# Optimization experiments

Measured on AMD Instinct MI355X. Metric: run time of the kernel, lower is better.

## Reference

```python
import jax, jax.numpy as jnp
import numpy as np

NUM_HEADS = 16
EPS = 1e-6
ROPE_THETA = 10000.0


def _rmsnorm_fp32(x, w):
    # RMSNorm computed in fp32, scale by learned weight (per head_dim)
    xf = x.astype(jnp.float32)
    var = jnp.mean(xf * xf, axis=-1, keepdims=True)
    return (xf * jax.lax.rsqrt(var + EPS) * w.astype(jnp.float32)).astype(x.dtype)


def _rope_3d_angles(T, H, W, head_dim):
    # split head_dim across (t,h,w) axes; all parts even
    dh = 2 * ((head_dim // 3) // 2)
    dw = dh
    dt = head_dim - dh - dw

    def axis_ang(L, d):
        inv = 1.0 / (ROPE_THETA ** (jnp.arange(0, d, 2, dtype=jnp.float32) / d))
        return jnp.arange(L, dtype=jnp.float32)[:, None] * inv[None, :]  # [L, d//2]

    at = axis_ang(T, dt)  # [T, dt/2]
    ah = axis_ang(H, dh)  # [H, dh/2]
    aw = axis_ang(W, dw)  # [W, dw/2]
    # broadcast to [T,H,W, head_dim//2] then flatten to [N, head_dim//2]
    at_g = jnp.broadcast_to(at[:, None, None, :], (T, H, W, dt // 2))
    ah_g = jnp.broadcast_to(ah[None, :, None, :], (T, H, W, dh // 2))
    aw_g = jnp.broadcast_to(aw[None, None, :, :], (T, H, W, dw // 2))
    ang = jnp.concatenate([at_g, ah_g, aw_g], axis=-1).reshape(T * H * W, head_dim // 2)
    return jnp.cos(ang), jnp.sin(ang)


def _apply_rope(x, cos, sin):
    # x: [B,Hh,N,D]; cos/sin: [N, D/2]; interleaved complex-pair rotation
    xr = x[..., 0::2]
    xi = x[..., 1::2]
    c = cos[None, None, :, :]
    s = sin[None, None, :, :]
    out_r = xr * c - xi * s
    out_i = xr * s + xi * c
    return jnp.stack([out_r, out_i], axis=-1).reshape(x.shape)


def setup_inputs() -> dict:
    key = jax.random.key(0)
    ks = jax.random.split(key, 7)
    dim, hd = 2048, 128
    x = jax.random.normal(ks[0], (1, 2048, dim), dtype=jnp.float32)
    qkv_w = jax.random.normal(ks[1], (3 * dim, dim), dtype=jnp.float32) * (dim ** -0.5)
    qkv_b = jax.random.normal(ks[2], (3 * dim,), dtype=jnp.float32) * 0.02
    proj_w = jax.random.normal(ks[3], (dim, dim), dtype=jnp.float32) * (dim ** -0.5)
    proj_b = jax.random.normal(ks[4], (dim,), dtype=jnp.float32) * 0.02
    q_norm_w = jnp.ones((hd,), dtype=jnp.float32)
    k_norm_w = jnp.ones((hd,), dtype=jnp.float32)
    return {"x": x, "qkv_w": qkv_w, "qkv_b": qkv_b, "proj_w": proj_w,
            "proj_b": proj_b, "q_norm_w": q_norm_w, "k_norm_w": k_norm_w,
            "t_dim": 8, "h_dim": 16, "w_dim": 16}


def reference(x, qkv_w, qkv_b, proj_w, proj_b, q_norm_w, k_norm_w, t_dim, h_dim, w_dim):
    B, N, C = x.shape
    Hh = NUM_HEADS
    D = C // Hh
    scale = D ** -0.5
    # QKV projection (torch Linear: x @ W.T + b)
    qkv = x @ qkv_w.T + qkv_b                      # [B,N,3C]
    qkv = qkv.reshape(B, N, 3, Hh, D).transpose(2, 0, 3, 1, 4)  # [3,B,Hh,N,D]
    q, k, v = qkv[0], qkv[1], qkv[2]
    q = _rmsnorm_fp32(q, q_norm_w)
    k = _rmsnorm_fp32(k, k_norm_w)
    cos, sin = _rope_3d_angles(t_dim, h_dim, w_dim, D)
    q = _apply_rope(q, cos, sin)
    k = _apply_rope(k, cos, sin)
    # SDPA (non-causal)
    scores = jnp.einsum('bhqd,bhkd->bhqk', q, k) * scale
    attn = jax.nn.softmax(scores, axis=-1)
    out = jnp.einsum('bhqk,bhkd->bhqd', attn, v)   # [B,Hh,N,D]
    out = out.transpose(0, 2, 1, 3).reshape(B, N, C)
    return out @ proj_w.T + proj_b
```

## Files before the change

### kernel.cpp

```cpp
#include <hip/hip_runtime.h>
#include <hip/hip_bf16.h>
#include <cstdint>
#include <cstddef>

typedef __attribute__((ext_vector_type(8))) short bf16x8;
typedef __attribute__((ext_vector_type(4))) float f32x4;
typedef __attribute__((ext_vector_type(16))) float f32x16;

#define AS1 __attribute__((address_space(1)))
#define AS3 __attribute__((address_space(3)))

__device__ __forceinline__ void gload_lds16(const void* g, void* l) {
  __builtin_amdgcn_global_load_lds((const AS1 void*)g, (AS3 void*)l, 16, 0, 0);
}

__device__ __forceinline__ unsigned short f2bf(float x) {
  __hip_bfloat16 h = __float2bfloat16(x);
  return __builtin_bit_cast(unsigned short, h);
}
__device__ __forceinline__ float bf2f(unsigned short u) {
  return __builtin_bit_cast(float, (unsigned int)u << 16);
}
__device__ __forceinline__ unsigned cvtpk(float a, float b) {
  unsigned r;
  asm("v_cvt_pk_bf16_f32 %0, %1, %2" : "=v"(r) : "v"(a), "v"(b));
  return r;
}
__device__ __forceinline__ void pswap(unsigned& x, unsigned& y) {
  asm volatile("v_permlane32_swap_b32 %0, %1" : "+v"(x), "+v"(y));
}

__global__ __launch_bounds__(256) void k_cvt_bf16(const float* __restrict__ in,
                                                  unsigned short* __restrict__ out,
                                                  int n4) {
  int i = blockIdx.x * 256 + threadIdx.x;
  const int stride = gridDim.x * 256;
  for (; i < n4; i += stride) {
    float4 v = reinterpret_cast<const float4*>(in)[i];
    ushort4 o;
    o.x = f2bf(v.x); o.y = f2bf(v.y); o.z = f2bf(v.z); o.w = f2bf(v.w);
    reinterpret_cast<ushort4*>(out)[i] = o;
  }
}

__global__ __launch_bounds__(256) void k_rope_tab(float* __restrict__ cosT,
                                                  float* __restrict__ sinT,
                                                  const int* __restrict__ hdim,
                                                  const int* __restrict__ wdim) {
  int idx = blockIdx.x * 256 + threadIdx.x;
  if (idx >= 2048 * 64) return;
  const int n = idx >> 6, j = idx & 63;
  const int H = *hdim, W = *wdim;
  const int w = n % W;
  const int rem = n / W;
  const int h = rem % H;
  const int t = rem / H;
  float pos, i2, d;
  if (j < 22)      { pos = (float)t; i2 = (float)(2 * j);        d = 44.f; }
  else if (j < 43) { pos = (float)h; i2 = (float)(2 * (j - 22)); d = 42.f; }
  else             { pos = (float)w; i2 = (float)(2 * (j - 43)); d = 42.f; }
  const float ang = pos * powf(10000.0f, -i2 / d);
  cosT[idx] = cosf(ang);
  sinT[idx] = sinf(ang);
}

__global__ __launch_bounds__(256, 2) void k_gemmQKV(const unsigned short* __restrict__ A,
                                                    const unsigned short* __restrict__ B,
                                                    const float* __restrict__ bias,
                                                    unsigned short* __restrict__ C,
                                                    int M, int N, int K) {
  __shared__ __align__(16) char lds[81920];
  const int tid = threadIdx.x;
  const int lane = tid & 63;
  const int wid = tid >> 6;
  const int wr = wid >> 1, wc = wid & 1;

  const int xcd = blockIdx.x & 7;
  const int t = blockIdx.x >> 3;
  const int bx = xcd * 4 + (t & 3);
  const int by = t >> 2;
  const int row0 = by * 128, col0 = bx * 192;
  const int NT = K >> 5;

  auto stageA = [&](int kcol0, char* slot) {
#pragma unroll
    for (int r = 0; r < 2; ++r) {
      const int off = r * 4096 + tid * 16;
      const int pair = off >> 7;
      const int un = (off & 127) ^ ((pair & 7) << 4);
      const int grow = pair * 2 + (un >> 6);
      gload_lds16(A + (size_t)(row0 + grow) * K + kcol0 + ((un & 63) >> 1),
                  slot + r * 4096 + wid * 1024);
    }
  };
  auto stageB = [&](int kcol0, char* slot) {
#pragma unroll
    for (int r = 0; r < 3; ++r) {
      const int off = r * 4096 + tid * 16;
      const int pair = off >> 7;
      const int un = (off & 127) ^ ((pair & 7) << 4);
      const int grow = pair * 2 + (un >> 6);
      gload_lds16(B + (size_t)(col0 + grow) * K + kcol0 + ((un & 63) >> 1),
                  slot + r * 4096 + wid * 1024);
    }
  };
  auto frag = [&](const char* slot, int r, int kb) -> bf16x8 {
    return *reinterpret_cast<const bf16x8*>(
        slot + (r >> 1) * 128 + ((((r & 1) << 6) + kb) ^ (((r >> 1) & 7) << 4)));
  };

  f32x4 acc[4][6];
#pragma unroll
  for (int i = 0; i < 4; ++i)
#pragma unroll
    for (int j = 0; j < 6; ++j) acc[i][j] = (f32x4){0.f, 0.f, 0.f, 0.f};

#pragma unroll
  for (int p = 0; p < 3; ++p) {
    stageA(p * 32, lds + p * 8192);
    stageB(p * 32, lds + 32768 + p * 12288);
  }
  asm volatile("s_waitcnt vmcnt(10)" ::: "memory");
  __builtin_amdgcn_s_barrier();

  const int kb = (lane >> 4) << 4;
  for (int j = 0; j < NT; ++j) {
    const char* baseA = lds + (j & 3) * 8192;
    const char* baseB = lds + 32768 + (j & 3) * 12288;
    bf16x8 af[4], bq[6];
#pragma unroll
    for (int fr = 0; fr < 4; ++fr) af[fr] = frag(baseA, wr * 64 + fr * 16 + (lane & 15), kb);
#pragma unroll
    for (int fc = 0; fc < 6; ++fc) bq[fc] = frag(baseB, wc * 96 + fc * 16 + (lane & 15), kb);

    const int jp = j + 3;
    if (jp < NT) {
      stageA(jp * 32, lds + (jp & 3) * 8192);
      stageB(jp * 32, lds + 32768 + (jp & 3) * 12288);
      asm volatile("s_waitcnt vmcnt(10)" ::: "memory");
    } else if (j + 2 < NT) {
      asm volatile("s_waitcnt vmcnt(5)" ::: "memory");
    } else if (j + 1 < NT) {
      asm volatile("s_waitcnt vmcnt(0)" ::: "memory");
    }
    if (j + 1 < NT) __builtin_amdgcn_s_barrier();

    __builtin_amdgcn_s_setprio(1);
#pragma unroll
    for (int fr = 0; fr < 4; ++fr)
#pragma unroll
      for (int fc = 0; fc < 6; ++fc)
        acc[fr][fc] = __builtin_amdgcn_mfma_f32_16x16x32_bf16(af[fr], bq[fc], acc[fr][fc], 0, 0, 0);
    __builtin_amdgcn_s_setprio(0);
  }

#pragma unroll
  for (int fr = 0; fr < 4; ++fr)
#pragma unroll
    for (int fc = 0; fc < 6; ++fc) {
      const int col = col0 + wc * 96 + fc * 16 + (lane & 15);
      const float bv = bias[col];
#pragma unroll
      for (int jj = 0; jj < 4; ++jj) {
        const int row = row0 + wr * 64 + fr * 16 + (lane >> 4) * 4 + jj;
        C[(size_t)row * N + col] = f2bf(acc[fr][fc][jj] + bv);
      }
    }
}

__global__ __launch_bounds__(256, 2) void k_gemmProj(const unsigned short* __restrict__ A,
                                                     const unsigned short* __restrict__ B,
                                                     float* __restrict__ Cp,
                                                     int M, int N, int K, int KS) {
  __shared__ __align__(16) char lds[65536];
  const int tid = threadIdx.x;
  const int lane = tid & 63;
  const int wid = tid >> 6;
  const int wr = wid >> 1, wc = wid & 1;
  const int row0 = blockIdx.y * 128;
  const int col0 = blockIdx.x * 128;
  const int k0 = blockIdx.z * KS;
  const int NT = KS >> 5;

  auto stageS = [&](const unsigned short* src, int grow0, int kcol0, char* slot) {
#pragma unroll
    for (int r = 0; r < 2; ++r) {
      const int off = r * 4096 + tid * 16;
      const int pair = off >> 7;
      const int un = (off & 127) ^ ((pair & 7) << 4);
      const int grow = pair * 2 + (un >> 6);
      gload_lds16(src + (size_t)(grow0 + grow) * K + kcol0 + ((un & 63) >> 1),
                  slot + r * 4096 + wid * 1024);
    }
  };
  auto frag = [&](const char* slot, int r, int kb) -> bf16x8 {
    return *reinterpret_cast<const bf16x8*>(
        slot + (r >> 1) * 128 + ((((r & 1) << 6) + kb) ^ (((r >> 1) & 7) << 4)));
  };

  f32x4 acc[4][4];
#pragma unroll
  for (int i = 0; i < 4; ++i)
#pragma unroll
    for (int j = 0; j < 4; ++j) acc[i][j] = (f32x4){0.f, 0.f, 0.f, 0.f};

#pragma unroll
  for (int p = 0; p < 3; ++p) {
    stageS(A, row0, k0 + p * 32, lds + p * 8192);
    stageS(B, col0, k0 + p * 32, lds + 32768 + p * 8192);
  }
  asm volatile("s_waitcnt vmcnt(8)" ::: "memory");
  __builtin_amdgcn_s_barrier();

  const int kb = (lane >> 4) << 4;
  for (int j = 0; j < NT; ++j) {
    const char* baseA = lds + (j & 3) * 8192;
    const char* baseB = lds + 32768 + (j & 3) * 8192;
    bf16x8 af[4], bq[4];
#pragma unroll
    for (int fr = 0; fr < 4; ++fr) af[fr] = frag(baseA, wr * 64 + fr * 16 + (lane & 15), kb);
#pragma unroll
    for (int fc = 0; fc < 4; ++fc) bq[fc] = frag(baseB, wc * 64 + fc * 16 + (lane & 15), kb);

    const int jp = j + 3;
    if (jp < NT) {
      stageS(A, row0, k0 + jp * 32, lds + (jp & 3) * 8192);
      stageS(B, col0, k0 + jp * 32, lds + 32768 + (jp & 3) * 8192);
      asm volatile("s_waitcnt vmcnt(8)" ::: "memory");
    } else if (j + 2 < NT) {
      asm volatile("s_waitcnt vmcnt(4)" ::: "memory");
    } else if (j + 1 < NT) {
      asm volatile("s_waitcnt vmcnt(0)" ::: "memory");
    }
    if (j + 1 < NT) __builtin_amdgcn_s_barrier();

    __builtin_amdgcn_s_setprio(1);
#pragma unroll
    for (int fr = 0; fr < 4; ++fr)
#pragma unroll
      for (int fc = 0; fc < 4; ++fc)
        acc[fr][fc] = __builtin_amdgcn_mfma_f32_16x16x32_bf16(af[fr], bq[fc], acc[fr][fc], 0, 0, 0);
    __builtin_amdgcn_s_setprio(0);
  }

  float* Cz = Cp + (size_t)blockIdx.z * M * N;
#pragma unroll
  for (int fr = 0; fr < 4; ++fr)
#pragma unroll
    for (int fc = 0; fc < 4; ++fc) {
      const int col = col0 + wc * 64 + fc * 16 + (lane & 15);
#pragma unroll
      for (int jj = 0; jj < 4; ++jj) {
        const int row = row0 + wr * 64 + fr * 16 + (lane >> 4) * 4 + jj;
        Cz[(size_t)row * N + col] = acc[fr][fc][jj];
      }
    }
}

__global__ __launch_bounds__(256) void k_addbias(const float* __restrict__ Cp,
                                                 const float* __restrict__ bias,
                                                 float* __restrict__ out) {
  const int i = blockIdx.x * 256 + threadIdx.x;
  const float4 a = reinterpret_cast<const float4*>(Cp)[i];
  const float4 b = reinterpret_cast<const float4*>(Cp + 2048ull * 2048)[i];
  const float4 bv = reinterpret_cast<const float4*>(bias)[i & 511];
  float4 o;
  o.x = a.x + b.x + bv.x; o.y = a.y + b.y + bv.y;
  o.z = a.z + b.z + bv.z; o.w = a.w + b.w + bv.w;
  reinterpret_cast<float4*>(out)[i] = o;
}

__global__ __launch_bounds__(256) void k_qk_post(const unsigned short* __restrict__ qkv,
                                                 const float* __restrict__ qw,
                                                 const float* __restrict__ kw,
                                                 const float* __restrict__ cosT,
                                                 const float* __restrict__ sinT,
                                                 unsigned short* __restrict__ qo,
                                                 unsigned short* __restrict__ ko) {
  const int lane = threadIdx.x & 63;
  const int wid = threadIdx.x >> 6;
  const int pair = blockIdx.x * 4 + wid;
  const int n = pair >> 4, h = pair & 15;
  const float c = cosT[n * 64 + lane];
  const float s = sinT[n * 64 + lane];
#pragma unroll
  for (int sq = 0; sq < 2; ++sq) {
    const unsigned short* src = qkv + (size_t)n * 6144 + sq * 2048 + h * 128;
    const unsigned int vp = reinterpret_cast<const unsigned int*>(src)[lane];
    const float vx = bf2f((unsigned short)(vp & 0xffff));
    const float vy = bf2f((unsigned short)(vp >> 16));
    float ss = vx * vx + vy * vy;
#pragma unroll
    for (int m = 1; m < 64; m <<= 1) ss += __shfl_xor(ss, m, 64);
    const float r = rsqrtf(ss * (1.0f / 128.0f) + 1e-6f);
    float2 wv = reinterpret_cast<const float2*>(sq == 0 ? qw : kw)[lane];
    const float xr = vx * r * wv.x;
    const float xi = vy * r * wv.y;
    float orr = xr * c - xi * s;
    float oi  = xr * s + xi * c;
    if (sq == 0) { orr *= 0.08838834764831845f; oi *= 0.08838834764831845f; }
    unsigned short* dst = (sq == 0 ? qo : ko) + ((size_t)h * 2048 + n) * 128 + 2 * lane;
    const unsigned int pk = (unsigned int)f2bf(orr) | ((unsigned int)f2bf(oi) << 16);
    *reinterpret_cast<unsigned int*>(dst) = pk;
  }
}

__global__ __launch_bounds__(256) void k_v_tr(const unsigned short* __restrict__ qkv,
                                              unsigned short* __restrict__ vt2) {
  __shared__ __align__(16) unsigned short tile[64][136];
  const int h = blockIdx.y;
  const int n0 = blockIdx.x * 64;
  const int t = threadIdx.x;
  {
    const int row = t >> 2;
    const int c0 = (t & 3) * 32;
    const unsigned short* src = qkv + (size_t)(n0 + row) * 6144 + 4096 + h * 128 + c0;
#pragma unroll
    for (int j = 0; j < 32; j += 8)
      *reinterpret_cast<bf16x8*>(&tile[row][c0 + j]) =
          *reinterpret_cast<const bf16x8*>(src + j);
  }
  __syncthreads();
#pragma unroll
  for (int g4 = 0; g4 < 4; ++g4) {
    const int g = g4 * 256 + t;
    const int c = g >> 8;
    const int dblk = (g >> 6) & 3;
    const int p = g & 63;
    const int d = dblk * 32 + (p & 31);
    const int hi = p >> 5;
    bf16x8 o;
#pragma unroll
    for (int e = 0; e < 8; ++e) o[e] = (short)tile[c * 16 + hi * 8 + e][d];
    const size_t oidx = ((((size_t)h * 128 + (n0 >> 4) + c) * 4 + dblk) * 64 + p) * 8;
    *reinterpret_cast<bf16x8*>(vt2 + oidx) = o;
  }
}

__global__ __launch_bounds__(256) void k_fattn(const unsigned short* __restrict__ q,
                                               const unsigned short* __restrict__ k,
                                               const unsigned short* __restrict__ vt2,
                                               unsigned short* __restrict__ Onorm,
                                               float* __restrict__ lseb) {
  __shared__ __align__(16) unsigned short Ks[2][64 * 128];
  __shared__ __align__(16) unsigned short Vs[2][64 * 128];
  const int lane = threadIdx.x & 63;
  const int wid = threadIdx.x >> 6;
  const int hi2 = lane >> 5;
  const int ql = lane & 31;
  const int bid = blockIdx.x;
  const int h = bid & 15;
  const int qb = (bid >> 4) & 15;
  const int ksp = bid >> 8;
  const int q0 = qb * 128 + wid * 32;
  const int kbase = ksp * 1024;

  auto stageK = [&](int buf, int kt2) {
#pragma unroll
    for (int r = 0; r < 4; ++r) {
      const int off = r * 4096 + (wid * 64 + lane) * 16;
      const int row = off >> 8;
      const int colb = (off & 255) ^ ((row & 15) << 4);
      gload_lds16(k + ((size_t)h * 2048 + kbase + kt2 * 64 + row) * 128 + (colb >> 1),
                  (char*)Ks[buf] + r * 4096 + wid * 1024);
    }
  };
  auto stageV = [&](int buf, int kt2) {
    const unsigned short* vbase = vt2 + ((size_t)h * 128 + (kbase >> 4) + kt2 * 4) * 2048;
#pragma unroll
    for (int r = 0; r < 4; ++r)
      gload_lds16(vbase + r * 2048 + (wid * 64 + lane) * 8,
                  (char*)Vs[buf] + r * 4096 + wid * 1024);
  };

  bf16x8 qf[8];
  {
    const unsigned short* qp = q + ((size_t)h * 2048 + q0 + ql) * 128 + hi2 * 8;
#pragma unroll
    for (int c = 0; c < 8; ++c) qf[c] = *reinterpret_cast<const bf16x8*>(qp + c * 16);
  }
  f32x16 O[4];
#pragma unroll
  for (int i = 0; i < 4; ++i)
#pragma unroll
    for (int j = 0; j < 16; ++j) O[i][j] = 0.f;
  float m = -1e30f, l = 0.f;

  stageK(0, 0);
  stageV(0, 0);
  asm volatile("s_waitcnt vmcnt(0)" ::: "memory");
  __builtin_amdgcn_s_barrier();

  const int kswz = (lane & 15) << 4;
  for (int kt = 0; kt < 16; ++kt) {
    const int cur = kt & 1;
    const bool pf = (kt + 1 < 16);
    if (pf) { stageK(cur ^ 1, kt + 1); stageV(cur ^ 1, kt + 1); }

    f32x16 s0, s1;
#pragma unroll
    for (int j = 0; j < 16; ++j) { s0[j] = 0.f; s1[j] = 0.f; }
    __builtin_amdgcn_s_setprio(1);
#pragma unroll
    for (int c = 0; c < 8; ++c) {
      bf16x8 a0 = *reinterpret_cast<const bf16x8*>(
          (const char*)Ks[cur] + ql * 256 + ((c * 32 + hi2 * 16) ^ kswz));
      s0 = __builtin_amdgcn_mfma_f32_32x32x16_bf16(a0, qf[c], s0, 0, 0, 0);
    }
#pragma unroll
    for (int c = 0; c < 8; ++c) {
      bf16x8 a1 = *reinterpret_cast<const bf16x8*>(
          (const char*)Ks[cur] + (32 + ql) * 256 + ((c * 32 + hi2 * 16) ^ kswz));
      s1 = __builtin_amdgcn_mfma_f32_32x32x16_bf16(a1, qf[c], s1, 0, 0, 0);
    }
    __builtin_amdgcn_s_setprio(0);

    float mt = s0[0];
#pragma unroll
    for (int j = 1; j < 16; ++j) mt = fmaxf(mt, s0[j]);
#pragma unroll
    for (int j = 0; j < 16; ++j) mt = fmaxf(mt, s1[j]);
    mt = fmaxf(mt, __shfl_xor(mt, 32, 64));

    if (!__all(mt <= m + 8.0f)) {
      const float mn = fmaxf(m, mt);
      const float al = __expf(m - mn);
      m = mn;
      l *= al;
#pragma unroll
      for (int i = 0; i < 4; ++i)
#pragma unroll
        for (int j = 0; j < 16; ++j) O[i][j] *= al;
    }
    float rs = 0.f;
#pragma unroll
    for (int j = 0; j < 16; ++j) {
      s0[j] = __expf(s0[j] - m); rs += s0[j];
      s1[j] = __expf(s1[j] - m); rs += s1[j];
    }
    rs += __shfl_xor(rs, 32, 64);
    l += rs;

    bf16x8 pfr[4];
#pragma unroll
    for (int half = 0; half < 2; ++half) {
      const f32x16& sv = half ? s1 : s0;
      unsigned a[8];
#pragma unroll
      for (int j2 = 0; j2 < 8; ++j2) a[j2] = cvtpk(sv[2 * j2], sv[2 * j2 + 1]);
      pswap(a[0], a[2]);
      pswap(a[1], a[3]);
      pswap(a[4], a[6]);
      pswap(a[5], a[7]);
      union { uint4 u; bf16x8 v; } p0, p1;
      p0.u.x = a[0]; p0.u.y = a[1]; p0.u.z = a[2]; p0.u.w = a[3];
      p1.u.x = a[4]; p1.u.y = a[5]; p1.u.z = a[6]; p1.u.w = a[7];
      pfr[half * 2 + 0] = p0.v;
      pfr[half * 2 + 1] = p1.v;
    }

    __builtin_amdgcn_s_setprio(1);
#pragma unroll
    for (int dblk = 0; dblk < 4; ++dblk) {
#pragma unroll
      for (int c2 = 0; c2 < 4; ++c2) {
        bf16x8 va = *reinterpret_cast<const bf16x8*>(
            (const char*)Vs[cur] + ((c2 * 4 + dblk) * 64 + lane) * 16);
        O[dblk] = __builtin_amdgcn_mfma_f32_32x32x16_bf16(va, pfr[c2], O[dblk], 0, 0, 0);
      }
    }
    __builtin_amdgcn_s_setprio(0);

    if (pf) {
      asm volatile("s_waitcnt vmcnt(0)" ::: "memory");
      __builtin_amdgcn_s_barrier();
    }
  }

  const float rl = 1.0f / l;
  const int n = q0 + ql;
  unsigned short* ob = Onorm + (((size_t)(ksp * 16 + h) * 2048) + n) * 128;
#pragma unroll
  for (int dblk = 0; dblk < 4; ++dblk)
#pragma unroll
    for (int a = 0; a < 4; ++a) {
      uint2 w;
      w.x = (unsigned)f2bf(O[dblk][a * 4 + 0] * rl) | ((unsigned)f2bf(O[dblk][a * 4 + 1] * rl) << 16);
      w.y = (unsigned)f2bf(O[dblk][a * 4 + 2] * rl) | ((unsigned)f2bf(O[dblk][a * 4 + 3] * rl) << 16);
      *reinterpret_cast<uint2*>(ob + dblk * 32 + a * 8 + hi2 * 4) = w;
    }
  if (hi2 == 0)
    lseb[(size_t)(ksp * 16 + h) * 2048 + n] = m + logf(l);
}

__global__ __launch_bounds__(256) void k_merge(const unsigned short* __restrict__ Onorm,
                                               const float* __restrict__ lseb,
                                               unsigned short* __restrict__ att) {
  const int idx = blockIdx.x * 256 + threadIdx.x;
  const int n = idx >> 8;
  const int r = idx & 255;
  const int h = r >> 4;
  const int d0 = (r & 15) * 8;
  const float l0 = lseb[(size_t)h * 2048 + n];
  const float l1 = lseb[(size_t)(16 + h) * 2048 + n];
  const float M = fmaxf(l0, l1);
  float w0 = __expf(l0 - M), w1 = __expf(l1 - M);
  const float inv = 1.0f / (w0 + w1);
  w0 *= inv; w1 *= inv;
  const bf16x8 o0 = *reinterpret_cast<const bf16x8*>(
      Onorm + ((size_t)h * 2048 + n) * 128 + d0);
  const bf16x8 o1 = *reinterpret_cast<const bf16x8*>(
      Onorm + ((size_t)(16 + h) * 2048 + n) * 128 + d0);
  bf16x8 o;
#pragma unroll
  for (int e = 0; e < 8; ++e)
    o[e] = (short)f2bf(bf2f((unsigned short)o0[e]) * w0 + bf2f((unsigned short)o1[e]) * w1);
  *reinterpret_cast<bf16x8*>(att + (size_t)n * 2048 + h * 128 + d0) = o;
}

extern "C" void kernel_launch(void* const* d_in, const int* in_sizes, int n_in,
                              void* d_out, int out_size, void* d_ws, size_t ws_size,
                              hipStream_t stream) {
  (void)in_sizes; (void)n_in; (void)out_size; (void)ws_size;
  const float* x      = (const float*)d_in[0];
  const float* qkv_w  = (const float*)d_in[1];
  const float* qkv_b  = (const float*)d_in[2];
  const float* proj_w = (const float*)d_in[3];
  const float* proj_b = (const float*)d_in[4];
  const float* q_nw   = (const float*)d_in[5];
  const float* k_nw   = (const float*)d_in[6];
  const int* h_dim    = (const int*)d_in[8];
  const int* w_dim    = (const int*)d_in[9];
  float* out = (float*)d_out;

  char* ws = (char*)d_ws;
  size_t off = 0;
  auto carve = [&](size_t bytes) -> void* {
    void* p = ws + off;
    off += (bytes + 255) & ~(size_t)255;
    return p;
  };
  unsigned short* x_bf   = (unsigned short*)carve(2048ull * 2048 * 2);
  unsigned short* w1_bf  = (unsigned short*)carve(6144ull * 2048 * 2);
  unsigned short* w2_bf  = (unsigned short*)carve(2048ull * 2048 * 2);
  unsigned short* qkvb   = (unsigned short*)carve(2048ull * 6144 * 2);
  unsigned short* q_bf   = (unsigned short*)carve(16ull * 2048 * 128 * 2);
  unsigned short* k_bf   = (unsigned short*)carve(16ull * 2048 * 128 * 2);
  unsigned short* vt2_bf = (unsigned short*)carve(16ull * 2048 * 128 * 2);
  unsigned short* att_bf = (unsigned short*)carve(2048ull * 2048 * 2);
  unsigned short* on_bf  = (unsigned short*)carve(2ull * 16 * 2048 * 128 * 2);
  float*          lseb   = (float*)carve(2ull * 16 * 2048 * 4);
  float*          projp  = (float*)carve(2ull * 2048 * 2048 * 4);
  float*          cosT   = (float*)carve(2048ull * 64 * 4);
  float*          sinT   = (float*)carve(2048ull * 64 * 4);

  hipLaunchKernelGGL(k_cvt_bf16, dim3(2048), dim3(256), 0, stream, x, x_bf, 2048 * 2048 / 4);
  hipLaunchKernelGGL(k_cvt_bf16, dim3(2048), dim3(256), 0, stream, qkv_w, w1_bf, 6144 * 2048 / 4);
  hipLaunchKernelGGL(k_cvt_bf16, dim3(2048), dim3(256), 0, stream, proj_w, w2_bf, 2048 * 2048 / 4);
  hipLaunchKernelGGL(k_rope_tab, dim3(512), dim3(256), 0, stream, cosT, sinT, h_dim, w_dim);
  hipLaunchKernelGGL(k_gemmQKV, dim3(512), dim3(256), 0, stream,
                     x_bf, w1_bf, qkv_b, qkvb, 2048, 6144, 2048);
  hipLaunchKernelGGL(k_qk_post, dim3(8192), dim3(256), 0, stream,
                     qkvb, q_nw, k_nw, cosT, sinT, q_bf, k_bf);
  hipLaunchKernelGGL(k_v_tr, dim3(32, 16), dim3(256), 0, stream, qkvb, vt2_bf);
  hipLaunchKernelGGL(k_fattn, dim3(512), dim3(256), 0, stream,
                     q_bf, k_bf, vt2_bf, on_bf, lseb);
  hipLaunchKernelGGL(k_merge, dim3(2048), dim3(256), 0, stream, on_bf, lseb, att_bf);
  hipLaunchKernelGGL(k_gemmProj, dim3(16, 16, 2), dim3(256), 0, stream,
                     att_bf, w2_bf, projp, 2048, 2048, 2048, 1024);
  hipLaunchKernelGGL(k_addbias, dim3(4096), dim3(256), 0, stream, projp, proj_b, out);
}
```

Before: 179.1 us.

## Double-buffer MFMA fragments in registers to overlap LDS reads with compute

Both GEMM kernels (QKV and output projection) now keep two register sets of A/B fragments. The main loop is unrolled by two, so the LDS fragment reads for the next k-step are issued before the MFMAs of the current step. This is meant to hide LDS read latency behind matrix-core work. In exchange it roughly doubles the fragment register footprint, which could cut occupancy under launch_bounds(256,2), and the loop now assumes NT is even.

```diff
diff --git a/kernel.cpp b/kernel.cpp
--- a/kernel.cpp
+++ b/kernel.cpp
@@ -76,9 +76,9 @@
   const int wr = wid >> 1, wc = wid & 1;
 
   const int xcd = blockIdx.x & 7;
-  const int t = blockIdx.x >> 3;
-  const int bx = xcd * 4 + (t & 3);
-  const int by = t >> 2;
+  const int t0 = blockIdx.x >> 3;
+  const int bx = xcd * 4 + (t0 & 3);
+  const int by = t0 >> 2;
   const int row0 = by * 128, col0 = bx * 192;
   const int NT = K >> 5;
 
@@ -124,34 +124,69 @@
   __builtin_amdgcn_s_barrier();
 
   const int kb = (lane >> 4) << 4;
-  for (int j = 0; j < NT; ++j) {
-    const char* baseA = lds + (j & 3) * 8192;
-    const char* baseB = lds + 32768 + (j & 3) * 12288;
-    bf16x8 af[4], bq[6];
-#pragma unroll
-    for (int fr = 0; fr < 4; ++fr) af[fr] = frag(baseA, wr * 64 + fr * 16 + (lane & 15), kb);
-#pragma unroll
-    for (int fc = 0; fc < 6; ++fc) bq[fc] = frag(baseB, wc * 96 + fc * 16 + (lane & 15), kb);
-
-    const int jp = j + 3;
-    if (jp < NT) {
-      stageA(jp * 32, lds + (jp & 3) * 8192);
-      stageB(jp * 32, lds + 32768 + (jp & 3) * 12288);
-      asm volatile("s_waitcnt vmcnt(10)" ::: "memory");
-    } else if (j + 2 < NT) {
-      asm volatile("s_waitcnt vmcnt(5)" ::: "memory");
-    } else if (j + 1 < NT) {
-      asm volatile("s_waitcnt vmcnt(0)" ::: "memory");
-    }
-    if (j + 1 < NT) __builtin_amdgcn_s_barrier();
-
-    __builtin_amdgcn_s_setprio(1);
-#pragma unroll
-    for (int fr = 0; fr < 4; ++fr)
-#pragma unroll
-      for (int fc = 0; fc < 6; ++fc)
-        acc[fr][fc] = __builtin_amdgcn_mfma_f32_16x16x32_bf16(af[fr], bq[fc], acc[fr][fc], 0, 0, 0);
-    __builtin_amdgcn_s_setprio(0);
+  bf16x8 afA[4], bqA[6], afB[4], bqB[6];
+#pragma unroll
+  for (int fr = 0; fr < 4; ++fr) afA[fr] = frag(lds, wr * 64 + fr * 16 + (lane & 15), kb);
+#pragma unroll
+  for (int fc = 0; fc < 6; ++fc) bqA[fc] = frag(lds + 32768, wc * 96 + fc * 16 + (lane & 15), kb);
+
+  for (int j = 0; j < NT; j += 2) {
+    {
+      const int jp = j + 3;
+      if (jp < NT) {
+        stageA(jp * 32, lds + (jp & 3) * 8192);
+        stageB(jp * 32, lds + 32768 + (jp & 3) * 12288);
+        asm volatile("s_waitcnt vmcnt(10)" ::: "memory");
+      } else if (j + 2 < NT) {
+        asm volatile("s_waitcnt vmcnt(5)" ::: "memory");
+      } else {
+        asm volatile("s_waitcnt vmcnt(0)" ::: "memory");
+      }
+      __builtin_amdgcn_s_barrier();
+      const char* bA = lds + ((j + 1) & 3) * 8192;
+      const char* bB = lds + 32768 + ((j + 1) & 3) * 12288;
+#pragma unroll
+      for (int fr = 0; fr < 4; ++fr) afB[fr] = frag(bA, wr * 64 + fr * 16 + (lane & 15), kb);
+#pragma unroll
+      for (int fc = 0; fc < 6; ++fc) bqB[fc] = frag(bB, wc * 96 + fc * 16 + (lane & 15), kb);
+      __builtin_amdgcn_s_setprio(1);
+#pragma unroll
+      for (int fr = 0; fr < 4; ++fr)
+#pragma unroll
+        for (int fc = 0; fc < 6; ++fc)
+          acc[fr][fc] = __builtin_amdgcn_mfma_f32_16x16x32_bf16(afA[fr], bqA[fc], acc[fr][fc], 0, 0, 0);
+      __builtin_amdgcn_s_setprio(0);
+    }
+    {
+      const int t = j + 1;
+      const int jp = t + 3;
+      const bool more = (t + 1 < NT);
+      if (jp < NT) {
+        stageA(jp * 32, lds + (jp & 3) * 8192);
+        stageB(jp * 32, lds + 32768 + (jp & 3) * 12288);
+        asm volatile("s_waitcnt vmcnt(10)" ::: "memory");
+      } else if (t + 2 < NT) {
+        asm volatile("s_waitcnt vmcnt(5)" ::: "memory");
+      } else if (more) {
+        asm volatile("s_waitcnt vmcnt(0)" ::: "memory");
+      }
+      if (more) {
+        __builtin_amdgcn_s_barrier();
+        const char* bA = lds + ((t + 1) & 3) * 8192;
+        const char* bB = lds + 32768 + ((t + 1) & 3) * 12288;
+#pragma unroll
+        for (int fr = 0; fr < 4; ++fr) afA[fr] = frag(bA, wr * 64 + fr * 16 + (lane & 15), kb);
+#pragma unroll
+        for (int fc = 0; fc < 6; ++fc) bqA[fc] = frag(bB, wc * 96 + fc * 16 + (lane & 15), kb);
+      }
+      __builtin_amdgcn_s_setprio(1);
+#pragma unroll
+      for (int fr = 0; fr < 4; ++fr)
+#pragma unroll
+        for (int fc = 0; fc < 6; ++fc)
+          acc[fr][fc] = __builtin_amdgcn_mfma_f32_16x16x32_bf16(afB[fr], bqB[fc], acc[fr][fc], 0, 0, 0);
+      __builtin_amdgcn_s_setprio(0);
+    }
   }
 
 #pragma unroll
@@ -213,34 +248,69 @@
   __builtin_amdgcn_s_barrier();
 
   const int kb = (lane >> 4) << 4;
-  for (int j = 0; j < NT; ++j) {
-    const char* baseA = lds + (j & 3) * 8192;
-    const char* baseB = lds + 32768 + (j & 3) * 8192;
-    bf16x8 af[4], bq[4];
-#pragma unroll
-    for (int fr = 0; fr < 4; ++fr) af[fr] = frag(baseA, wr * 64 + fr * 16 + (lane & 15), kb);
-#pragma unroll
-    for (int fc = 0; fc < 4; ++fc) bq[fc] = frag(baseB, wc * 64 + fc * 16 + (lane & 15), kb);
-
-    const int jp = j + 3;
-    if (jp < NT) {
-      stageS(A, row0, k0 + jp * 32, lds + (jp & 3) * 8192);
-      stageS(B, col0, k0 + jp * 32, lds + 32768 + (jp & 3) * 8192);
-      asm volatile("s_waitcnt vmcnt(8)" ::: "memory");
-    } else if (j + 2 < NT) {
-      asm volatile("s_waitcnt vmcnt(4)" ::: "memory");
-    } else if (j + 1 < NT) {
-      asm volatile("s_waitcnt vmcnt(0)" ::: "memory");
-    }
-    if (j + 1 < NT) __builtin_amdgcn_s_barrier();
-
-    __builtin_amdgcn_s_setprio(1);
-#pragma unroll
-    for (int fr = 0; fr < 4; ++fr)
-#pragma unroll
-      for (int fc = 0; fc < 4; ++fc)
-        acc[fr][fc] = __builtin_amdgcn_mfma_f32_16x16x32_bf16(af[fr], bq[fc], acc[fr][fc], 0, 0, 0);
-    __builtin_amdgcn_s_setprio(0);
+  bf16x8 afA[4], bqA[4], afB[4], bqB[4];
+#pragma unroll
+  for (int fr = 0; fr < 4; ++fr) afA[fr] = frag(lds, wr * 64 + fr * 16 + (lane & 15), kb);
+#pragma unroll
+  for (int fc = 0; fc < 4; ++fc) bqA[fc] = frag(lds + 32768, wc * 64 + fc * 16 + (lane & 15), kb);
+
+  for (int j = 0; j < NT; j += 2) {
+    {
+      const int jp = j + 3;
+      if (jp < NT) {
+        stageS(A, row0, k0 + jp * 32, lds + (jp & 3) * 8192);
+        stageS(B, col0, k0 + jp * 32, lds + 32768 + (jp & 3) * 8192);
+        asm volatile("s_waitcnt vmcnt(8)" ::: "memory");
+      } else if (j + 2 < NT) {
+        asm volatile("s_waitcnt vmcnt(4)" ::: "memory");
+      } else {
+        asm volatile("s_waitcnt vmcnt(0)" ::: "memory");
+      }
+      __builtin_amdgcn_s_barrier();
+      const char* bA = lds + ((j + 1) & 3) * 8192;
+      const char* bB = lds + 32768 + ((j + 1) & 3) * 8192;
+#pragma unroll
+      for (int fr = 0; fr < 4; ++fr) afB[fr] = frag(bA, wr * 64 + fr * 16 + (lane & 15), kb);
+#pragma unroll
+      for (int fc = 0; fc < 4; ++fc) bqB[fc] = frag(bB, wc * 64 + fc * 16 + (lane & 15), kb);
+      __builtin_amdgcn_s_setprio(1);
+#pragma unroll
+      for (int fr = 0; fr < 4; ++fr)
+#pragma unroll
+        for (int fc = 0; fc < 4; ++fc)
+          acc[fr][fc] = __builtin_amdgcn_mfma_f32_16x16x32_bf16(afA[fr], bqA[fc], acc[fr][fc], 0, 0, 0);
+      __builtin_amdgcn_s_setprio(0);
+    }
+    {
+      const int t = j + 1;
+      const int jp = t + 3;
+      const bool more = (t + 1 < NT);
+      if (jp < NT) {
+        stageS(A, row0, k0 + jp * 32, lds + (jp & 3) * 8192);
+        stageS(B, col0, k0 + jp * 32, lds + 32768 + (jp & 3) * 8192);
+        asm volatile("s_waitcnt vmcnt(8)" ::: "memory");
+      } else if (t + 2 < NT) {
+        asm volatile("s_waitcnt vmcnt(4)" ::: "memory");
+      } else if (more) {
+        asm volatile("s_waitcnt vmcnt(0)" ::: "memory");
+      }
+      if (more) {
+        __builtin_amdgcn_s_barrier();
+        const char* bA = lds + ((t + 1) & 3) * 8192;
+        const char* bB = lds + 32768 + ((t + 1) & 3) * 8192;
+#pragma unroll
+        for (int fr = 0; fr < 4; ++fr) afA[fr] = frag(bA, wr * 64 + fr * 16 + (lane & 15), kb);
+#pragma unroll
+        for (int fc = 0; fc < 4; ++fc) bqA[fc] = frag(bB, wc * 64 + fc * 16 + (lane & 15), kb);
+      }
+      __builtin_amdgcn_s_setprio(1);
+#pragma unroll
+      for (int fr = 0; fr < 4; ++fr)
+#pragma unroll
+        for (int fc = 0; fc < 4; ++fc)
+          acc[fr][fc] = __builtin_amdgcn_mfma_f32_16x16x32_bf16(afB[fr], bqB[fc], acc[fr][fc], 0, 0, 0);
+      __builtin_amdgcn_s_setprio(0);
+    }
   }
 
   float* Cz = Cp + (size_t)blockIdx.z * M * N;
```

Result: no change. 178.4 us (-0.4%).

## Split attention keys four ways, single-buffer K tile, fuse weight conversions

Applied to the files above, without the earlier changes.

Flash attention now splits the key range into four 512-key chunks instead of two, doubling the grid to 1024 blocks, and the merge kernel combines four partial outputs using log-sum-exp weights. The K tile in shared memory becomes single-buffered, with a barrier after the QK MFMAs before prefetching the next tile. This lowers LDS use per block and may let more blocks share a CU. The three fp32-to-bf16 conversion launches are merged into one kernel. The cost is twice the partial-output traffic, a merge that reads twice as much, and K prefetch that can no longer overlap the QK compute.

```diff
diff --git a/kernel.cpp b/kernel.cpp
--- a/kernel.cpp
+++ b/kernel.cpp
@@ -30,16 +30,24 @@
   asm volatile("v_permlane32_swap_b32 %0, %1" : "+v"(x), "+v"(y));
 }
 
-__global__ __launch_bounds__(256) void k_cvt_bf16(const float* __restrict__ in,
-                                                  unsigned short* __restrict__ out,
-                                                  int n4) {
-  int i = blockIdx.x * 256 + threadIdx.x;
+__global__ __launch_bounds__(256) void k_cvt3(const float* __restrict__ a, unsigned short* __restrict__ ao, int na4,
+                                              const float* __restrict__ b, unsigned short* __restrict__ bo, int nb4,
+                                              const float* __restrict__ c, unsigned short* __restrict__ co, int nc4) {
   const int stride = gridDim.x * 256;
-  for (; i < n4; i += stride) {
-    float4 v = reinterpret_cast<const float4*>(in)[i];
-    ushort4 o;
-    o.x = f2bf(v.x); o.y = f2bf(v.y); o.z = f2bf(v.z); o.w = f2bf(v.w);
-    reinterpret_cast<ushort4*>(out)[i] = o;
+  for (int i = blockIdx.x * 256 + threadIdx.x; i < na4; i += stride) {
+    float4 v = reinterpret_cast<const float4*>(a)[i];
+    ushort4 o; o.x = f2bf(v.x); o.y = f2bf(v.y); o.z = f2bf(v.z); o.w = f2bf(v.w);
+    reinterpret_cast<ushort4*>(ao)[i] = o;
+  }
+  for (int i = blockIdx.x * 256 + threadIdx.x; i < nb4; i += stride) {
+    float4 v = reinterpret_cast<const float4*>(b)[i];
+    ushort4 o; o.x = f2bf(v.x); o.y = f2bf(v.y); o.z = f2bf(v.z); o.w = f2bf(v.w);
+    reinterpret_cast<ushort4*>(bo)[i] = o;
+  }
+  for (int i = blockIdx.x * 256 + threadIdx.x; i < nc4; i += stride) {
+    float4 v = reinterpret_cast<const float4*>(c)[i];
+    ushort4 o; o.x = f2bf(v.x); o.y = f2bf(v.y); o.z = f2bf(v.z); o.w = f2bf(v.w);
+    reinterpret_cast<ushort4*>(co)[i] = o;
   }
 }
 
@@ -76,9 +84,9 @@
   const int wr = wid >> 1, wc = wid & 1;
 
   const int xcd = blockIdx.x & 7;
-  const int t = blockIdx.x >> 3;
-  const int bx = xcd * 4 + (t & 3);
-  const int by = t >> 2;
+  const int t0 = blockIdx.x >> 3;
+  const int bx = xcd * 4 + (t0 & 3);
+  const int by = t0 >> 2;
   const int row0 = by * 128, col0 = bx * 192;
   const int NT = K >> 5;
 
@@ -342,7 +350,7 @@
                                                const unsigned short* __restrict__ vt2,
                                                unsigned short* __restrict__ Onorm,
                                                float* __restrict__ lseb) {
-  __shared__ __align__(16) unsigned short Ks[2][64 * 128];
+  __shared__ __align__(16) unsigned short Ks[64 * 128];
   __shared__ __align__(16) unsigned short Vs[2][64 * 128];
   const int lane = threadIdx.x & 63;
   const int wid = threadIdx.x >> 6;
@@ -353,16 +361,16 @@
   const int qb = (bid >> 4) & 15;
   const int ksp = bid >> 8;
   const int q0 = qb * 128 + wid * 32;
-  const int kbase = ksp * 1024;
-
-  auto stageK = [&](int buf, int kt2) {
+  const int kbase = ksp * 512;
+
+  auto stageK = [&](int kt2) {
 #pragma unroll
     for (int r = 0; r < 4; ++r) {
       const int off = r * 4096 + (wid * 64 + lane) * 16;
       const int row = off >> 8;
       const int colb = (off & 255) ^ ((row & 15) << 4);
       gload_lds16(k + ((size_t)h * 2048 + kbase + kt2 * 64 + row) * 128 + (colb >> 1),
-                  (char*)Ks[buf] + r * 4096 + wid * 1024);
+                  (char*)Ks + r * 4096 + wid * 1024);
     }
   };
   auto stageV = [&](int buf, int kt2) {
@@ -386,16 +394,15 @@
     for (int j = 0; j < 16; ++j) O[i][j] = 0.f;
   float m = -1e30f, l = 0.f;
 
-  stageK(0, 0);
+  stageK(0);
   stageV(0, 0);
   asm volatile("s_waitcnt vmcnt(0)" ::: "memory");
   __builtin_amdgcn_s_barrier();
 
   const int kswz = (lane & 15) << 4;
-  for (int kt = 0; kt < 16; ++kt) {
+  for (int kt = 0; kt < 8; ++kt) {
     const int cur = kt & 1;
-    const bool pf = (kt + 1 < 16);
-    if (pf) { stageK(cur ^ 1, kt + 1); stageV(cur ^ 1, kt + 1); }
+    const bool pf = (kt + 1 < 8);
 
     f32x16 s0, s1;
 #pragma unroll
@@ -404,16 +411,18 @@
 #pragma unroll
     for (int c = 0; c < 8; ++c) {
       bf16x8 a0 = *reinterpret_cast<const bf16x8*>(
-          (const char*)Ks[cur] + ql * 256 + ((c * 32 + hi2 * 16) ^ kswz));
+          (const char*)Ks + ql * 256 + ((c * 32 + hi2 * 16) ^ kswz));
       s0 = __builtin_amdgcn_mfma_f32_32x32x16_bf16(a0, qf[c], s0, 0, 0, 0);
     }
 #pragma unroll
     for (int c = 0; c < 8; ++c) {
       bf16x8 a1 = *reinterpret_cast<const bf16x8*>(
-          (const char*)Ks[cur] + (32 + ql) * 256 + ((c * 32 + hi2 * 16) ^ kswz));
+          (const char*)Ks + (32 + ql) * 256 + ((c * 32 + hi2 * 16) ^ kswz));
       s1 = __builtin_amdgcn_mfma_f32_32x32x16_bf16(a1, qf[c], s1, 0, 0, 0);
     }
     __builtin_amdgcn_s_setprio(0);
+    __builtin_amdgcn_s_barrier();
+    if (pf) { stageK(kt + 1); stageV(cur ^ 1, kt + 1); }
 
     float mt = s0[0];
 #pragma unroll
@@ -501,20 +510,28 @@
   const int r = idx & 255;
   const int h = r >> 4;
   const int d0 = (r & 15) * 8;
-  const float l0 = lseb[(size_t)h * 2048 + n];
-  const float l1 = lseb[(size_t)(16 + h) * 2048 + n];
-  const float M = fmaxf(l0, l1);
-  float w0 = __expf(l0 - M), w1 = __expf(l1 - M);
-  const float inv = 1.0f / (w0 + w1);
-  w0 *= inv; w1 *= inv;
-  const bf16x8 o0 = *reinterpret_cast<const bf16x8*>(
-      Onorm + ((size_t)h * 2048 + n) * 128 + d0);
-  const bf16x8 o1 = *reinterpret_cast<const bf16x8*>(
-      Onorm + ((size_t)(16 + h) * 2048 + n) * 128 + d0);
+  float ls[4];
+#pragma unroll
+  for (int p = 0; p < 4; ++p) ls[p] = lseb[(size_t)(p * 16 + h) * 2048 + n];
+  float M = fmaxf(fmaxf(ls[0], ls[1]), fmaxf(ls[2], ls[3]));
+  float wsum = 0.f, w[4];
+#pragma unroll
+  for (int p = 0; p < 4; ++p) { w[p] = __expf(ls[p] - M); wsum += w[p]; }
+  const float inv = 1.0f / wsum;
+  float acc[8];
+#pragma unroll
+  for (int e = 0; e < 8; ++e) acc[e] = 0.f;
+#pragma unroll
+  for (int p = 0; p < 4; ++p) {
+    const bf16x8 o = *reinterpret_cast<const bf16x8*>(
+        Onorm + ((size_t)(p * 16 + h) * 2048 + n) * 128 + d0);
+    const float wp = w[p] * inv;
+#pragma unroll
+    for (int e = 0; e < 8; ++e) acc[e] += bf2f((unsigned short)o[e]) * wp;
+  }
   bf16x8 o;
 #pragma unroll
-  for (int e = 0; e < 8; ++e)
-    o[e] = (short)f2bf(bf2f((unsigned short)o0[e]) * w0 + bf2f((unsigned short)o1[e]) * w1);
+  for (int e = 0; e < 8; ++e) o[e] = (short)f2bf(acc[e]);
   *reinterpret_cast<bf16x8*>(att + (size_t)n * 2048 + h * 128 + d0) = o;
 }
 
@@ -548,22 +565,23 @@
   unsigned short* k_bf   = (unsigned short*)carve(16ull * 2048 * 128 * 2);
   unsigned short* vt2_bf = (unsigned short*)carve(16ull * 2048 * 128 * 2);
   unsigned short* att_bf = (unsigned short*)carve(2048ull * 2048 * 2);
-  unsigned short* on_bf  = (unsigned short*)carve(2ull * 16 * 2048 * 128 * 2);
-  float*          lseb   = (float*)carve(2ull * 16 * 2048 * 4);
+  unsigned short* on_bf  = (unsigned short*)carve(4ull * 16 * 2048 * 128 * 2);
+  float*          lseb   = (float*)carve(4ull * 16 * 2048 * 4);
   float*          projp  = (float*)carve(2ull * 2048 * 2048 * 4);
   float*          cosT   = (float*)carve(2048ull * 64 * 4);
   float*          sinT   = (float*)carve(2048ull * 64 * 4);
 
-  hipLaunchKernelGGL(k_cvt_bf16, dim3(2048), dim3(256), 0, stream, x, x_bf, 2048 * 2048 / 4);
-  hipLaunchKernelGGL(k_cvt_bf16, dim3(2048), dim3(256), 0, stream, qkv_w, w1_bf, 6144 * 2048 / 4);
-  hipLaunchKernelGGL(k_cvt_bf16, dim3(2048), dim3(256), 0, stream, proj_w, w2_bf, 2048 * 2048 / 4);
+  hipLaunchKernelGGL(k_cvt3, dim3(2048), dim3(256), 0, stream,
+                     x, x_bf, 2048 * 2048 / 4,
+                     qkv_w, w1_bf, 6144 * 2048 / 4,
+                     proj_w, w2_bf, 2048 * 2048 / 4);
   hipLaunchKernelGGL(k_rope_tab, dim3(512), dim3(256), 0, stream, cosT, sinT, h_dim, w_dim);
   hipLaunchKernelGGL(k_gemmQKV, dim3(512), dim3(256), 0, stream,
                      x_bf, w1_bf, qkv_b, qkvb, 2048, 6144, 2048);
   hipLaunchKernelGGL(k_qk_post, dim3(8192), dim3(256), 0, stream,
                      qkvb, q_nw, k_nw, cosT, sinT, q_bf, k_bf);
   hipLaunchKernelGGL(k_v_tr, dim3(32, 16), dim3(256), 0, stream, qkvb, vt2_bf);
-  hipLaunchKernelGGL(k_fattn, dim3(512), dim3(256), 0, stream,
+  hipLaunchKernelGGL(k_fattn, dim3(1024), dim3(256), 0, stream,
                      q_bf, k_bf, vt2_bf, on_bf, lseb);
   hipLaunchKernelGGL(k_merge, dim3(2048), dim3(256), 0, stream, on_bf, lseb, att_bf);
   hipLaunchKernelGGL(k_gemmProj, dim3(16, 16, 2), dim3(256), 0, stream,
```

After: 202.3 us. 12.9% more time.
